# Kernel tuning notes

Hardware: AMD Instinct MI355X
Metric: run time of the kernel (lower is better)

## Reference

```python
import jax, jax.numpy as jnp
import numpy as np

D_MODEL = 1024
N_HEADS = 16
D_HEAD = D_MODEL // N_HEADS
SCALE = 1.0 / np.sqrt(D_HEAD)


def setup_inputs() -> dict:
    key = jax.random.key(0)
    ks = jax.random.split(key, 5)
    B, S = 2, 2048
    x = jax.random.normal(ks[0], (B, S, D_MODEL), dtype=jnp.float32)
    # torch F.linear weights have shape (d_out, d_in); kaiming-uniform-ish init
    bound = 1.0 / np.sqrt(D_MODEL)
    Wq = jax.random.uniform(ks[1], (D_MODEL, D_MODEL), jnp.float32, -bound, bound)
    Wk = jax.random.uniform(ks[2], (D_MODEL, D_MODEL), jnp.float32, -bound, bound)
    Wv = jax.random.uniform(ks[3], (D_MODEL, D_MODEL), jnp.float32, -bound, bound)
    Wo = jax.random.uniform(ks[4], (D_MODEL, D_MODEL), jnp.float32, -bound, bound)
    return {"x": x, "Wq": Wq, "Wk": Wk, "Wv": Wv, "Wo": Wo}


def reference(x, Wq, Wk, Wv, Wo):
    B, S, _ = x.shape
    # F.linear(x, W) = x @ W.T; reshape to [B, H, S, Dh]
    def proj(W):
        return (x @ W.T).reshape(B, S, N_HEADS, D_HEAD).transpose(0, 2, 1, 3)
    Q, K, V = proj(Wq), proj(Wk), proj(Wv)
    # scores [B, H, S, S]
    attn = jnp.einsum('bhqd,bhkd->bhqk', Q, K) * SCALE
    causal = jnp.tril(jnp.ones((S, S), dtype=bool))
    attn = jnp.where(causal, attn, -jnp.inf)
    attn = jax.nn.softmax(attn, axis=-1)
    out = jnp.einsum('bhqk,bhkd->bhqd', attn, V)
    out = out.transpose(0, 2, 1, 3).reshape(B, S, D_MODEL)
    return out @ Wo.T
```

## Files before the change

### kernel.cpp

```cpp
#include <hip/hip_runtime.h>


typedef __attribute__((ext_vector_type(8))) short short8;
typedef __attribute__((ext_vector_type(4))) float f32x4;
typedef __attribute__((ext_vector_type(4))) _Float16 half4;

#if __has_builtin(__builtin_amdgcn_exp2f)
#define EXP2F(x) __builtin_amdgcn_exp2f(x)
#else
#define EXP2F(x) exp2f(x)
#endif

__device__ __forceinline__ unsigned short f2bf(float f) {
  unsigned int x = __float_as_uint(f);
  x += 0x7fffu + ((x >> 16) & 1u);
  return (unsigned short)(x >> 16);
}

__device__ __forceinline__ void gload16(const void* g, void* l) {
  __builtin_amdgcn_global_load_lds(
      (const __attribute__((address_space(1))) void*)g,
      (__attribute__((address_space(3))) void*)l, 16, 0, 0);
}

__device__ __forceinline__ int swz64(int row, int sc) {
  return row * 64 + ((((sc >> 3) ^ (row & 7)) << 3) | (sc & 7));
}

__global__ void cast5_kernel(const float* __restrict__ x, const float* __restrict__ wq,
                             const float* __restrict__ wk, const float* __restrict__ wv,
                             const float* __restrict__ wo,
                             unsigned short* __restrict__ xb, unsigned short* __restrict__ wqb,
                             unsigned short* __restrict__ wkb, unsigned short* __restrict__ wvb,
                             unsigned short* __restrict__ wob) {
  const float* in; unsigned short* out; int n4; float sc = 1.f;
  switch (blockIdx.y) {
    case 0: in = x;  out = xb;  n4 = 1048576; break;
    case 1: in = wq; out = wqb; n4 = 262144; sc = 0.18033688011112042f; break;
    case 2: in = wk; out = wkb; n4 = 262144; break;
    case 3: in = wv; out = wvb; n4 = 262144; break;
    default: in = wo; out = wob; n4 = 262144; break;
  }
  int i = blockIdx.x * 256 + threadIdx.x;
  if (i >= n4) return;
  float4 v = ((const float4*)in)[i];
  union { unsigned short u[4]; uint2 p; } o;
  o.u[0] = f2bf(v.x * sc); o.u[1] = f2bf(v.y * sc);
  o.u[2] = f2bf(v.z * sc); o.u[3] = f2bf(v.w * sc);
  ((uint2*)out)[i] = o.p;
}

#define GK 1024

__global__ __launch_bounds__(256) void gemm_qkv_kernel(
    const unsigned short* __restrict__ X,
    const unsigned short* __restrict__ Wq,
    const unsigned short* __restrict__ Wk,
    const unsigned short* __restrict__ Wv,
    unsigned short* __restrict__ Qo,
    unsigned short* __restrict__ Ko,
    _Float16* __restrict__ Vt) {
  __shared__ unsigned short As[128 * 32];
  __shared__ unsigned short Bs[128 * 32];
  int mb = blockIdx.x;
  int nbT = blockIdx.y;
  int sel = nbT >> 3, nb = nbT & 7;
  const unsigned short* W = sel == 0 ? Wq : (sel == 1 ? Wk : Wv);

  int tid = threadIdx.x;
  int w = tid >> 6, l = tid & 63, quad = l >> 4, lo = l & 15;
  int wm = (w >> 1) * 64, wn = (w & 1) * 64;

  f32x4 acc[4][4];
#pragma unroll
  for (int i = 0; i < 4; i++)
#pragma unroll
    for (int j = 0; j < 4; j++) acc[i][j] = (f32x4){0.f, 0.f, 0.f, 0.f};

  for (int k0 = 0; k0 < GK; k0 += 32) {
    __syncthreads();
#pragma unroll
    for (int i = 0; i < 2; i++) {
      int c = i * 256 + tid;
      gload16(X + (size_t)(mb * 128 + (c >> 2)) * GK + k0 + (c & 3) * 8,
              (char*)As + c * 16);
      gload16(W + (size_t)(nb * 128 + (c >> 2)) * GK + k0 + (c & 3) * 8,
              (char*)Bs + c * 16);
    }
    __syncthreads();
    short8 a[4], b[4];
#pragma unroll
    for (int mi = 0; mi < 4; mi++)
      a[mi] = *(const short8*)&As[(wm + mi * 16 + lo) * 32 + quad * 8];
#pragma unroll
    for (int ni = 0; ni < 4; ni++)
      b[ni] = *(const short8*)&Bs[(wn + ni * 16 + lo) * 32 + quad * 8];
#pragma unroll
    for (int mi = 0; mi < 4; mi++)
#pragma unroll
      for (int ni = 0; ni < 4; ni++)
        acc[mi][ni] = __builtin_amdgcn_mfma_f32_16x16x32_bf16(a[mi], b[ni],
                                                              acc[mi][ni], 0, 0, 0);
  }
  if (sel == 2) {
#pragma unroll
    for (int mi = 0; mi < 4; mi++)
#pragma unroll
      for (int ni = 0; ni < 4; ni++) {
        int row0 = mb * 128 + wm + mi * 16 + quad * 4;
        int col = nb * 128 + wn + ni * 16 + lo;
        int bb = row0 >> 11, ss = row0 & 2047;
        int hh = col >> 6, dd = col & 63;
        half4 v;
#pragma unroll
        for (int r = 0; r < 4; r++) v[r] = (_Float16)acc[mi][ni][r];
        *(half4*)&Vt[((size_t)((bb * 16 + hh) * 64 + dd)) * 2048 + ss] = v;
      }
  } else {
    unsigned short* C = sel == 0 ? Qo : Ko;
#pragma unroll
    for (int mi = 0; mi < 4; mi++)
#pragma unroll
      for (int ni = 0; ni < 4; ni++)
#pragma unroll
        for (int r = 0; r < 4; r++) {
          int row = mb * 128 + wm + mi * 16 + quad * 4 + r;
          int col = nb * 128 + wn + ni * 16 + lo;
          C[(size_t)row * 1024 + col] = f2bf(acc[mi][ni][r]);
        }
  }
}

__global__ __launch_bounds__(256) void gemm_out_kernel(
    const unsigned short* __restrict__ A,
    const unsigned short* __restrict__ W,
    float* __restrict__ C) {
  __shared__ unsigned short As[128 * 32];
  __shared__ unsigned short Bs[128 * 32];
  int mb = blockIdx.x, nb = blockIdx.y;
  int tid = threadIdx.x;
  int w = tid >> 6, l = tid & 63, quad = l >> 4, lo = l & 15;
  int wm = (w >> 1) * 64, wn = (w & 1) * 64;

  f32x4 acc[4][4];
#pragma unroll
  for (int i = 0; i < 4; i++)
#pragma unroll
    for (int j = 0; j < 4; j++) acc[i][j] = (f32x4){0.f, 0.f, 0.f, 0.f};

  for (int k0 = 0; k0 < GK; k0 += 32) {
    __syncthreads();
#pragma unroll
    for (int i = 0; i < 2; i++) {
      int c = i * 256 + tid;
      gload16(A + (size_t)(mb * 128 + (c >> 2)) * GK + k0 + (c & 3) * 8,
              (char*)As + c * 16);
      gload16(W + (size_t)(nb * 128 + (c >> 2)) * GK + k0 + (c & 3) * 8,
              (char*)Bs + c * 16);
    }
    __syncthreads();
    short8 a[4], b[4];
#pragma unroll
    for (int mi = 0; mi < 4; mi++)
      a[mi] = *(const short8*)&As[(wm + mi * 16 + lo) * 32 + quad * 8];
#pragma unroll
    for (int ni = 0; ni < 4; ni++)
      b[ni] = *(const short8*)&Bs[(wn + ni * 16 + lo) * 32 + quad * 8];
#pragma unroll
    for (int mi = 0; mi < 4; mi++)
#pragma unroll
      for (int ni = 0; ni < 4; ni++)
        acc[mi][ni] = __builtin_amdgcn_mfma_f32_16x16x32_bf16(a[mi], b[ni],
                                                              acc[mi][ni], 0, 0, 0);
  }
#pragma unroll
  for (int mi = 0; mi < 4; mi++)
#pragma unroll
    for (int ni = 0; ni < 4; ni++)
#pragma unroll
      for (int r = 0; r < 4; r++) {
        int row = mb * 128 + wm + mi * 16 + quad * 4 + r;
        int col = nb * 128 + wn + ni * 16 + lo;
        C[(size_t)row * 1024 + col] = acc[mi][ni][r];
      }
}

__global__ __launch_bounds__(256) void attn_kernel(
    const unsigned short* __restrict__ Q,
    const unsigned short* __restrict__ K,
    const _Float16* __restrict__ Vt,
    unsigned short* __restrict__ O) {
  const int S = 2048, DM = 1024;
  __shared__ unsigned short Qs[128 * 64];
  __shared__ unsigned short Ks[64 * 64];
  __shared__ _Float16 Vts[64 * 64];

  int id = blockIdx.x;
  int qidx = id >> 5, bh = id & 31;
  int qt = (qidx < 8) ? qidx : 23 - qidx;
  int b = bh >> 4, h = bh & 15;
  size_t base = (size_t)b * S * DM + h * 64;
  size_t baseVt = (size_t)(bh * 64) * S;

  int tid = threadIdx.x;
  int w = tid >> 6, lane = tid & 63, quad = lane >> 4, lo = lane & 15;
  int qb_w = qt * 128 + w * 32;

#pragma unroll
  for (int j = 0; j < 4; j++) {
    int s_ = j * 256 + tid;
    int row = s_ >> 3, lc = (s_ & 7) ^ (row & 7);
    gload16(Q + base + (size_t)(qt * 128 + row) * DM + lc * 8, (char*)Qs + s_ * 16);
  }

  short8 qf[2][2];
  f32x4 oacc[2][4];
  float m_[2], l_[2];
#pragma unroll
  for (int s = 0; s < 2; s++) {
    m_[s] = -1e30f; l_[s] = 0.f;
#pragma unroll
    for (int ni = 0; ni < 4; ni++) oacc[s][ni] = (f32x4){0.f, 0.f, 0.f, 0.f};
  }

  int tend = 2 * qt + 2;
  for (int t = 0; t < tend; t++) {
    __syncthreads();
#pragma unroll
    for (int j = 0; j < 2; j++) {
      int s_ = j * 256 + tid;
      int row = s_ >> 3, lc = (s_ & 7) ^ (row & 7);
      gload16(K + base + (size_t)(t * 64 + row) * DM + lc * 8, (char*)Ks + s_ * 16);
      gload16(Vt + baseVt + (size_t)row * S + t * 64 + lc * 8, (char*)Vts + s_ * 16);
    }
    if (t == 0) {
#pragma unroll
      for (int s = 0; s < 2; s++)
#pragma unroll
        for (int d = 0; d < 2; d++)
          qf[s][d] = *(const short8*)&Qs[swz64(w * 32 + s * 16 + lo, d * 32 + quad * 8)];
    }
    __syncthreads();

    f32x4 st[2][4];
#pragma unroll
    for (int s = 0; s < 2; s++)
#pragma unroll
      for (int kvt = 0; kvt < 4; kvt++) st[s][kvt] = (f32x4){0.f, 0.f, 0.f, 0.f};
#pragma unroll
    for (int kvt = 0; kvt < 4; kvt++)
#pragma unroll
      for (int d = 0; d < 2; d++) {
        short8 kf = *(const short8*)&Ks[swz64(kvt * 16 + lo, d * 32 + quad * 8)];
        st[0][kvt] = __builtin_amdgcn_mfma_f32_16x16x32_bf16(kf, qf[0][d], st[0][kvt], 0, 0, 0);
        st[1][kvt] = __builtin_amdgcn_mfma_f32_16x16x32_bf16(kf, qf[1][d], st[1][kvt], 0, 0, 0);
      }

    half4 pf[2][4];
#pragma unroll
    for (int s = 0; s < 2; s++) {
      int qrow0 = qb_w + s * 16;
      float z[4][4];
#pragma unroll
      for (int kvt = 0; kvt < 4; kvt++)
#pragma unroll
        for (int r = 0; r < 4; r++) z[kvt][r] = st[s][kvt][r];
      if (t * 64 + 63 > qrow0) {
        int qg = qrow0 + lo;
#pragma unroll
        for (int kvt = 0; kvt < 4; kvt++)
#pragma unroll
          for (int r = 0; r < 4; r++) {
            int kv = t * 64 + kvt * 16 + quad * 4 + r;
            if (kv > qg) z[kvt][r] = -1e30f;
          }
      }
      float mx = z[0][0];
#pragma unroll
      for (int kvt = 0; kvt < 4; kvt++)
#pragma unroll
        for (int r = 0; r < 4; r++) mx = fmaxf(mx, z[kvt][r]);
      mx = fmaxf(mx, __shfl_xor(mx, 16));
      mx = fmaxf(mx, __shfl_xor(mx, 32));
      float mnew = fmaxf(m_[s], mx);
      float alpha = EXP2F(m_[s] - mnew);
      m_[s] = mnew;
      float rs = 0.f;
#pragma unroll
      for (int kvt = 0; kvt < 4; kvt++)
#pragma unroll
        for (int r = 0; r < 4; r++) {
          float p = EXP2F(z[kvt][r] - mnew);
          z[kvt][r] = p;
          rs += p;
        }
      rs += __shfl_xor(rs, 16);
      rs += __shfl_xor(rs, 32);
      l_[s] = l_[s] * alpha + rs;
#pragma unroll
      for (int kvt = 0; kvt < 4; kvt++) {
        half4 p4;
#pragma unroll
        for (int r = 0; r < 4; r++) p4[r] = (_Float16)z[kvt][r];
        pf[s][kvt] = p4;
      }
      float ab[4];
#pragma unroll
      for (int r = 0; r < 4; r++) ab[r] = __shfl(alpha, (lane & 48) + quad * 4 + r);
#pragma unroll
      for (int ni = 0; ni < 4; ni++)
#pragma unroll
        for (int r = 0; r < 4; r++) oacc[s][ni][r] *= ab[r];
    }

#pragma unroll
    for (int kvt = 0; kvt < 4; kvt++) {
      half4 vf[4];
#pragma unroll
      for (int ni = 0; ni < 4; ni++)
        vf[ni] = *(const half4*)&Vts[swz64(ni * 16 + lo, kvt * 16 + quad * 4)];
#pragma unroll
      for (int s = 0; s < 2; s++)
#pragma unroll
        for (int ni = 0; ni < 4; ni++)
          oacc[s][ni] = __builtin_amdgcn_mfma_f32_16x16x16f16(pf[s][kvt], vf[ni],
                                                              oacc[s][ni], 0, 0, 0);
    }
  }

#pragma unroll
  for (int s = 0; s < 2; s++) {
    float inv[4];
#pragma unroll
    for (int r = 0; r < 4; r++)
      inv[r] = 1.0f / __shfl(l_[s], (lane & 48) + quad * 4 + r);
#pragma unroll
    for (int ni = 0; ni < 4; ni++)
#pragma unroll
      for (int r = 0; r < 4; r++) {
        int qg = qb_w + s * 16 + quad * 4 + r;
        O[base + (size_t)qg * DM + ni * 16 + lo] = f2bf(oacc[s][ni][r] * inv[r]);
      }
  }
}

extern "C" void kernel_launch(void* const* d_in, const int* in_sizes, int n_in,
                              void* d_out, int out_size, void* d_ws, size_t ws_size,
                              hipStream_t stream) {
  const float* x  = (const float*)d_in[0];
  const float* Wq = (const float*)d_in[1];
  const float* Wk = (const float*)d_in[2];
  const float* Wv = (const float*)d_in[3];
  const float* Wo = (const float*)d_in[4];
  float* out = (float*)d_out;
  char* ws = (char*)d_ws;

  unsigned short* Xb  = (unsigned short*)(ws);
  unsigned short* Wqb = (unsigned short*)(ws + (8ll  << 20));
  unsigned short* Wkb = (unsigned short*)(ws + (10ll << 20));
  unsigned short* Wvb = (unsigned short*)(ws + (12ll << 20));
  unsigned short* Wob = (unsigned short*)(ws + (14ll << 20));
  unsigned short* Qb  = (unsigned short*)(ws + (16ll << 20));
  unsigned short* Kb  = (unsigned short*)(ws + (24ll << 20));
  _Float16*       Vt  = (_Float16*)     (ws + (32ll << 20));
  unsigned short* Ob  = (unsigned short*)(ws + (40ll << 20));

  cast5_kernel<<<dim3(4096, 5), 256, 0, stream>>>(x, Wq, Wk, Wv, Wo,
                                                  Xb, Wqb, Wkb, Wvb, Wob);
  gemm_qkv_kernel<<<dim3(32, 24), 256, 0, stream>>>(Xb, Wqb, Wkb, Wvb, Qb, Kb, Vt);
  attn_kernel<<<512, 256, 0, stream>>>(Qb, Kb, Vt, Ob);
  gemm_out_kernel<<<dim3(32, 8), 256, 0, stream>>>(Ob, Wob, out);
}
```

Before: 215.9 us.

## Double-buffer K/V in attention, shrink query tiles, narrow output GEMM tiles

The attention kernel now uses 64-row query tiles with one 16-row slice per wave, giving 1024 blocks instead of 512. Blocks are ordered so the longest causal tiles start first. K and V^T tiles are double-buffered in LDS, so the next tile's global-to-LDS load is issued while the current one is computed, leaving one barrier per iteration. The output projection GEMM uses 128x64 tiles, doubling its grid to improve occupancy and CU coverage. Each block now does less work per byte, so per-block MFMA density is lower and Q fragment reuse drops.

Result: faster. 193.2 us (-10.5%).

```diff
diff --git a/kernel.cpp b/kernel.cpp
--- a/kernel.cpp
+++ b/kernel.cpp
@@ -136,15 +136,15 @@
     const unsigned short* __restrict__ W,
     float* __restrict__ C) {
   __shared__ unsigned short As[128 * 32];
-  __shared__ unsigned short Bs[128 * 32];
+  __shared__ unsigned short Bs[64 * 32];
   int mb = blockIdx.x, nb = blockIdx.y;
   int tid = threadIdx.x;
   int w = tid >> 6, l = tid & 63, quad = l >> 4, lo = l & 15;
-  int wm = (w >> 1) * 64, wn = (w & 1) * 64;
-
-  f32x4 acc[4][4];
-#pragma unroll
-  for (int i = 0; i < 4; i++)
+  int wm = w * 32;
+
+  f32x4 acc[2][4];
+#pragma unroll
+  for (int i = 0; i < 2; i++)
 #pragma unroll
     for (int j = 0; j < 4; j++) acc[i][j] = (f32x4){0.f, 0.f, 0.f, 0.f};
 
@@ -155,32 +155,32 @@
       int c = i * 256 + tid;
       gload16(A + (size_t)(mb * 128 + (c >> 2)) * GK + k0 + (c & 3) * 8,
               (char*)As + c * 16);
-      gload16(W + (size_t)(nb * 128 + (c >> 2)) * GK + k0 + (c & 3) * 8,
-              (char*)Bs + c * 16);
-    }
-    __syncthreads();
-    short8 a[4], b[4];
-#pragma unroll
-    for (int mi = 0; mi < 4; mi++)
+    }
+    gload16(W + (size_t)(nb * 64 + (tid >> 2)) * GK + k0 + (tid & 3) * 8,
+            (char*)Bs + tid * 16);
+    __syncthreads();
+    short8 a[2], b[4];
+#pragma unroll
+    for (int mi = 0; mi < 2; mi++)
       a[mi] = *(const short8*)&As[(wm + mi * 16 + lo) * 32 + quad * 8];
 #pragma unroll
     for (int ni = 0; ni < 4; ni++)
-      b[ni] = *(const short8*)&Bs[(wn + ni * 16 + lo) * 32 + quad * 8];
-#pragma unroll
-    for (int mi = 0; mi < 4; mi++)
+      b[ni] = *(const short8*)&Bs[(ni * 16 + lo) * 32 + quad * 8];
+#pragma unroll
+    for (int mi = 0; mi < 2; mi++)
 #pragma unroll
       for (int ni = 0; ni < 4; ni++)
         acc[mi][ni] = __builtin_amdgcn_mfma_f32_16x16x32_bf16(a[mi], b[ni],
                                                               acc[mi][ni], 0, 0, 0);
   }
 #pragma unroll
-  for (int mi = 0; mi < 4; mi++)
+  for (int mi = 0; mi < 2; mi++)
 #pragma unroll
     for (int ni = 0; ni < 4; ni++)
 #pragma unroll
       for (int r = 0; r < 4; r++) {
         int row = mb * 128 + wm + mi * 16 + quad * 4 + r;
-        int col = nb * 128 + wn + ni * 16 + lo;
+        int col = nb * 64 + ni * 16 + lo;
         C[(size_t)row * 1024 + col] = acc[mi][ni][r];
       }
 }
@@ -191,157 +191,145 @@
     const _Float16* __restrict__ Vt,
     unsigned short* __restrict__ O) {
   const int S = 2048, DM = 1024;
-  __shared__ unsigned short Qs[128 * 64];
-  __shared__ unsigned short Ks[64 * 64];
-  __shared__ _Float16 Vts[64 * 64];
+  __shared__ unsigned short Qs[64 * 64];
+  __shared__ unsigned short Ks[2][64 * 64];
+  __shared__ _Float16 Vts[2][64 * 64];
 
   int id = blockIdx.x;
-  int qidx = id >> 5, bh = id & 31;
-  int qt = (qidx < 8) ? qidx : 23 - qidx;
+  int bh = id & 31;
+  int qt = 31 - (id >> 5);
   int b = bh >> 4, h = bh & 15;
   size_t base = (size_t)b * S * DM + h * 64;
   size_t baseVt = (size_t)(bh * 64) * S;
 
   int tid = threadIdx.x;
   int w = tid >> 6, lane = tid & 63, quad = lane >> 4, lo = lane & 15;
-  int qb_w = qt * 128 + w * 32;
-
-#pragma unroll
-  for (int j = 0; j < 4; j++) {
+  int qrow0 = qt * 64 + w * 16;
+
+#pragma unroll
+  for (int j = 0; j < 2; j++) {
     int s_ = j * 256 + tid;
     int row = s_ >> 3, lc = (s_ & 7) ^ (row & 7);
-    gload16(Q + base + (size_t)(qt * 128 + row) * DM + lc * 8, (char*)Qs + s_ * 16);
-  }
-
-  short8 qf[2][2];
-  f32x4 oacc[2][4];
-  float m_[2], l_[2];
-#pragma unroll
-  for (int s = 0; s < 2; s++) {
-    m_[s] = -1e30f; l_[s] = 0.f;
-#pragma unroll
-    for (int ni = 0; ni < 4; ni++) oacc[s][ni] = (f32x4){0.f, 0.f, 0.f, 0.f};
-  }
-
-  int tend = 2 * qt + 2;
+    gload16(Q + base + (size_t)(qt * 64 + row) * DM + lc * 8, (char*)Qs + s_ * 16);
+  }
+#pragma unroll
+  for (int j = 0; j < 2; j++) {
+    int s_ = j * 256 + tid;
+    int row = s_ >> 3, lc = (s_ & 7) ^ (row & 7);
+    gload16(K + base + (size_t)row * DM + lc * 8, (char*)Ks[0] + s_ * 16);
+    gload16(Vt + baseVt + (size_t)row * S + lc * 8, (char*)Vts[0] + s_ * 16);
+  }
+
+  short8 qf[2];
+  f32x4 oacc[4];
+  float m_ = -1e30f, l_ = 0.f;
+#pragma unroll
+  for (int ni = 0; ni < 4; ni++) oacc[ni] = (f32x4){0.f, 0.f, 0.f, 0.f};
+
+  int tend = qt + 1;
   for (int t = 0; t < tend; t++) {
     __syncthreads();
-#pragma unroll
-    for (int j = 0; j < 2; j++) {
-      int s_ = j * 256 + tid;
-      int row = s_ >> 3, lc = (s_ & 7) ^ (row & 7);
-      gload16(K + base + (size_t)(t * 64 + row) * DM + lc * 8, (char*)Ks + s_ * 16);
-      gload16(Vt + baseVt + (size_t)row * S + t * 64 + lc * 8, (char*)Vts + s_ * 16);
+    if (t + 1 < tend) {
+      int tb = (t + 1) & 1;
+#pragma unroll
+      for (int j = 0; j < 2; j++) {
+        int s_ = j * 256 + tid;
+        int row = s_ >> 3, lc = (s_ & 7) ^ (row & 7);
+        gload16(K + base + (size_t)((t + 1) * 64 + row) * DM + lc * 8,
+                (char*)Ks[tb] + s_ * 16);
+        gload16(Vt + baseVt + (size_t)row * S + (t + 1) * 64 + lc * 8,
+                (char*)Vts[tb] + s_ * 16);
+      }
     }
     if (t == 0) {
 #pragma unroll
-      for (int s = 0; s < 2; s++)
-#pragma unroll
-        for (int d = 0; d < 2; d++)
-          qf[s][d] = *(const short8*)&Qs[swz64(w * 32 + s * 16 + lo, d * 32 + quad * 8)];
-    }
-    __syncthreads();
-
-    f32x4 st[2][4];
-#pragma unroll
-    for (int s = 0; s < 2; s++)
-#pragma unroll
-      for (int kvt = 0; kvt < 4; kvt++) st[s][kvt] = (f32x4){0.f, 0.f, 0.f, 0.f};
+      for (int d = 0; d < 2; d++)
+        qf[d] = *(const short8*)&Qs[swz64(w * 16 + lo, d * 32 + quad * 8)];
+    }
+    const unsigned short* ks = Ks[t & 1];
+    const _Float16* vs = Vts[t & 1];
+
+    f32x4 st[4];
+#pragma unroll
+    for (int kvt = 0; kvt < 4; kvt++) st[kvt] = (f32x4){0.f, 0.f, 0.f, 0.f};
 #pragma unroll
     for (int kvt = 0; kvt < 4; kvt++)
 #pragma unroll
       for (int d = 0; d < 2; d++) {
-        short8 kf = *(const short8*)&Ks[swz64(kvt * 16 + lo, d * 32 + quad * 8)];
-        st[0][kvt] = __builtin_amdgcn_mfma_f32_16x16x32_bf16(kf, qf[0][d], st[0][kvt], 0, 0, 0);
-        st[1][kvt] = __builtin_amdgcn_mfma_f32_16x16x32_bf16(kf, qf[1][d], st[1][kvt], 0, 0, 0);
-      }
-
-    half4 pf[2][4];
-#pragma unroll
-    for (int s = 0; s < 2; s++) {
-      int qrow0 = qb_w + s * 16;
-      float z[4][4];
+        short8 kf = *(const short8*)&ks[swz64(kvt * 16 + lo, d * 32 + quad * 8)];
+        st[kvt] = __builtin_amdgcn_mfma_f32_16x16x32_bf16(kf, qf[d], st[kvt], 0, 0, 0);
+      }
+
+    float z[4][4];
+#pragma unroll
+    for (int kvt = 0; kvt < 4; kvt++)
+#pragma unroll
+      for (int r = 0; r < 4; r++) z[kvt][r] = st[kvt][r];
+    if (t == tend - 1) {
+      int qg = qrow0 + lo;
 #pragma unroll
       for (int kvt = 0; kvt < 4; kvt++)
 #pragma unroll
-        for (int r = 0; r < 4; r++) z[kvt][r] = st[s][kvt][r];
-      if (t * 64 + 63 > qrow0) {
-        int qg = qrow0 + lo;
-#pragma unroll
-        for (int kvt = 0; kvt < 4; kvt++)
-#pragma unroll
-          for (int r = 0; r < 4; r++) {
-            int kv = t * 64 + kvt * 16 + quad * 4 + r;
-            if (kv > qg) z[kvt][r] = -1e30f;
-          }
-      }
-      float mx = z[0][0];
-#pragma unroll
-      for (int kvt = 0; kvt < 4; kvt++)
-#pragma unroll
-        for (int r = 0; r < 4; r++) mx = fmaxf(mx, z[kvt][r]);
-      mx = fmaxf(mx, __shfl_xor(mx, 16));
-      mx = fmaxf(mx, __shfl_xor(mx, 32));
-      float mnew = fmaxf(m_[s], mx);
-      float alpha = EXP2F(m_[s] - mnew);
-      m_[s] = mnew;
-      float rs = 0.f;
-#pragma unroll
-      for (int kvt = 0; kvt < 4; kvt++)
-#pragma unroll
         for (int r = 0; r < 4; r++) {
-          float p = EXP2F(z[kvt][r] - mnew);
-          z[kvt][r] = p;
-          rs += p;
+          int kv = t * 64 + kvt * 16 + quad * 4 + r;
+          if (kv > qg) z[kvt][r] = -1e30f;
         }
-      rs += __shfl_xor(rs, 16);
-      rs += __shfl_xor(rs, 32);
-      l_[s] = l_[s] * alpha + rs;
-#pragma unroll
-      for (int kvt = 0; kvt < 4; kvt++) {
-        half4 p4;
-#pragma unroll
-        for (int r = 0; r < 4; r++) p4[r] = (_Float16)z[kvt][r];
-        pf[s][kvt] = p4;
-      }
-      float ab[4];
-#pragma unroll
-      for (int r = 0; r < 4; r++) ab[r] = __shfl(alpha, (lane & 48) + quad * 4 + r);
-#pragma unroll
-      for (int ni = 0; ni < 4; ni++)
-#pragma unroll
-        for (int r = 0; r < 4; r++) oacc[s][ni][r] *= ab[r];
-    }
-
+    }
+
+    float mx = z[0][0];
+#pragma unroll
+    for (int kvt = 0; kvt < 4; kvt++)
+#pragma unroll
+      for (int r = 0; r < 4; r++) mx = fmaxf(mx, z[kvt][r]);
+    mx = fmaxf(mx, __shfl_xor(mx, 16));
+    mx = fmaxf(mx, __shfl_xor(mx, 32));
+    float mnew = fmaxf(m_, mx);
+    float alpha = EXP2F(m_ - mnew);
+    m_ = mnew;
+    float rs = 0.f;
+    half4 pf[4];
 #pragma unroll
     for (int kvt = 0; kvt < 4; kvt++) {
-      half4 vf[4];
-#pragma unroll
-      for (int ni = 0; ni < 4; ni++)
-        vf[ni] = *(const half4*)&Vts[swz64(ni * 16 + lo, kvt * 16 + quad * 4)];
-#pragma unroll
-      for (int s = 0; s < 2; s++)
-#pragma unroll
-        for (int ni = 0; ni < 4; ni++)
-          oacc[s][ni] = __builtin_amdgcn_mfma_f32_16x16x16f16(pf[s][kvt], vf[ni],
-                                                              oacc[s][ni], 0, 0, 0);
-    }
-  }
-
-#pragma unroll
-  for (int s = 0; s < 2; s++) {
-    float inv[4];
-#pragma unroll
-    for (int r = 0; r < 4; r++)
-      inv[r] = 1.0f / __shfl(l_[s], (lane & 48) + quad * 4 + r);
+      half4 p4;
+#pragma unroll
+      for (int r = 0; r < 4; r++) {
+        float p = EXP2F(z[kvt][r] - mnew);
+        p4[r] = (_Float16)p;
+        rs += p;
+      }
+      pf[kvt] = p4;
+    }
+    rs += __shfl_xor(rs, 16);
+    rs += __shfl_xor(rs, 32);
+    l_ = l_ * alpha + rs;
+    float ab[4];
+#pragma unroll
+    for (int r = 0; r < 4; r++) ab[r] = __shfl(alpha, (lane & 48) + quad * 4 + r);
 #pragma unroll
     for (int ni = 0; ni < 4; ni++)
 #pragma unroll
-      for (int r = 0; r < 4; r++) {
-        int qg = qb_w + s * 16 + quad * 4 + r;
-        O[base + (size_t)qg * DM + ni * 16 + lo] = f2bf(oacc[s][ni][r] * inv[r]);
-      }
-  }
+      for (int r = 0; r < 4; r++) oacc[ni][r] *= ab[r];
+
+#pragma unroll
+    for (int kvt = 0; kvt < 4; kvt++)
+#pragma unroll
+      for (int ni = 0; ni < 4; ni++) {
+        half4 vf = *(const half4*)&vs[swz64(ni * 16 + lo, kvt * 16 + quad * 4)];
+        oacc[ni] = __builtin_amdgcn_mfma_f32_16x16x16f16(pf[kvt], vf, oacc[ni], 0, 0, 0);
+      }
+  }
+
+  float inv[4];
+#pragma unroll
+  for (int r = 0; r < 4; r++)
+    inv[r] = 1.0f / __shfl(l_, (lane & 48) + quad * 4 + r);
+#pragma unroll
+  for (int ni = 0; ni < 4; ni++)
+#pragma unroll
+    for (int r = 0; r < 4; r++) {
+      int qg = qrow0 + quad * 4 + r;
+      O[base + (size_t)qg * DM + ni * 16 + lo] = f2bf(oacc[ni][r] * inv[r]);
+    }
 }
 
 extern "C" void kernel_launch(void* const* d_in, const int* in_sizes, int n_in,
@@ -368,6 +356,6 @@
   cast5_kernel<<<dim3(4096, 5), 256, 0, stream>>>(x, Wq, Wk, Wv, Wo,
                                                   Xb, Wqb, Wkb, Wvb, Wob);
   gemm_qkv_kernel<<<dim3(32, 24), 256, 0, stream>>>(Xb, Wqb, Wkb, Wvb, Qb, Kb, Vt);
-  attn_kernel<<<512, 256, 0, stream>>>(Qb, Kb, Vt, Ob);
-  gemm_out_kernel<<<dim3(32, 8), 256, 0, stream>>>(Ob, Wob, out);
-}
+  attn_kernel<<<1024, 256, 0, stream>>>(Qb, Kb, Vt, Ob);
+  gemm_out_kernel<<<dim3(32, 16), 256, 0, stream>>>(Ob, Wob, out);
+}
```
